# Optimization experiments

Hardware: AMD Instinct MI355X
Metric: run time of the kernel (lower is better)

The kernel has to match this reference:

```python
import jax, jax.numpy as jnp
import numpy as np

EMBED = 768
GH = 4        # heads per group
GD = 256      # group dim = GH * head_dim
NSTEPS = 3    # n_pde_steps
DT = 0.05
HJ_H = 0.05   # Heimburg-Jackson dispersion coefficient


def _sh(u, k):
    # shift field content along sequence axis (axis=1) by k with zero boundary
    if k == 0:
        return u
    z = jnp.zeros_like(u)
    if k > 0:
        return z.at[:, k:, :].set(u[:, :-k, :])
    return z.at[:, :k, :].set(u[:, -k:, :])


def _d1(u):
    return 0.5 * (_sh(u, -1) - _sh(u, 1))


def _d2(u):
    return _sh(u, -1) - 2.0 * u + _sh(u, 1)


def _d3(u):
    return 0.5 * (_sh(u, -2) - 2.0 * _sh(u, -1) + 2.0 * _sh(u, 1) - _sh(u, 2))


def _d4(u):
    return _sh(u, -2) - 4.0 * _sh(u, -1) + 6.0 * u - 4.0 * _sh(u, 1) + _sh(u, 2)


def _attn(x, qkv_w, qkv_b, ow, ob, nh):
    # standard causal multi-head attention on one head group
    B, T, D = x.shape
    hd = D // nh
    qkv = x @ qkv_w + qkv_b                      # (B,T,3D)
    q, k, v = jnp.split(qkv, 3, axis=-1)
    heads = lambda a: a.reshape(B, T, nh, hd).transpose(0, 2, 1, 3)
    q, k, v = heads(q), heads(k), heads(v)
    s = jnp.einsum('bhqd,bhkd->bhqk', q, k) * (1.0 / np.sqrt(hd))
    causal = jnp.tril(jnp.ones((T, T), dtype=bool))
    s = jnp.where(causal, s, jnp.asarray(-1e9, s.dtype))
    p = jax.nn.softmax(s, axis=-1)
    o = jnp.einsum('bhqk,bhkd->bhqd', p, v).transpose(0, 2, 1, 3).reshape(B, T, D)
    return o @ ow + ob


def _sine_gordon(u):
    # u_tt = u_xx - sin(u), semi-implicit Euler (leapfrog-like)
    w = jnp.zeros_like(u)
    for _ in range(NSTEPS):
        w = w + DT * (_d2(u) - jnp.sin(u))
        u = u + DT * w
    return u


def _kdv(u):
    # u_t = -6 u u_x - u_xxx, explicit Euler
    for _ in range(NSTEPS):
        u = u + DT * (-6.0 * u * _d1(u) - _d3(u))
    return u


def _hj(u):
    # Heimburg-Jackson: u_tt = d_xx((c0^2 + p u + q u^2) u) - h u_xxxx
    # with c0=1, p=-1, q=1
    w = jnp.zeros_like(u)
    for _ in range(NSTEPS):
        f = u - u * u + u * u * u
        w = w + DT * (_d2(f) - HJ_H * _d4(u))
        u = u + DT * w
    return u


def setup_inputs() -> dict:
    key = jax.random.key(0)
    ks = jax.random.split(key, 16)
    s = 0.02
    d, gd = EMBED, GD
    inp = {'x': jax.random.normal(ks[0], (4, 2048, d), dtype=jnp.float32)}
    inp['in_w'] = jax.random.normal(ks[1], (d, d), jnp.float32) * s
    inp['in_b'] = jnp.zeros((d,), jnp.float32)
    for i, n in enumerate(['sg', 'kdv', 'hj']):
        inp[n + '_qkv_w'] = jax.random.normal(ks[2 + 4 * i], (gd, 3 * gd), jnp.float32) * s
        inp[n + '_qkv_b'] = jnp.zeros((3 * gd,), jnp.float32)
        inp[n + '_out_w'] = jax.random.normal(ks[3 + 4 * i], (gd, gd), jnp.float32) * s
        inp[n + '_out_b'] = jnp.zeros((gd,), jnp.float32)
    inp['out_w'] = jax.random.normal(ks[14], (d, d), jnp.float32) * s
    inp['out_b'] = jnp.zeros((d,), jnp.float32)
    return inp


def reference(x, in_w, in_b,
              sg_qkv_w, sg_qkv_b, sg_out_w, sg_out_b,
              kdv_qkv_w, kdv_qkv_b, kdv_out_w, kdv_out_b,
              hj_qkv_w, hj_qkv_b, hj_out_w, hj_out_b,
              out_w, out_b):
    h = x @ in_w + in_b
    xg = jnp.split(h, [GD, 2 * GD], axis=-1)
    sg = _sine_gordon(_attn(xg[0], sg_qkv_w, sg_qkv_b, sg_out_w, sg_out_b, GH))
    kv = _kdv(_attn(xg[1], kdv_qkv_w, kdv_qkv_b, kdv_out_w, kdv_out_b, GH))
    hj = _hj(_attn(xg[2], hj_qkv_w, hj_qkv_b, hj_out_w, hj_out_b, GH))
    out = jnp.concatenate([sg, kv, hj], axis=-1)
    return out @ out_w + out_b
```

## Files before the change

kernel.cpp:

```cpp
#include <hip/hip_runtime.h>
#include <math.h>

#define B_   4
#define T_   2048
#define D_   768
#define M_   8192
#define GD_  256
#define NH_  4
#define HD_  64

typedef short  s16x8 __attribute__((ext_vector_type(8)));
typedef __bf16 bfx8  __attribute__((ext_vector_type(8)));
typedef float  fx4   __attribute__((ext_vector_type(4)));

#define LOG2E 1.44269504088896f
#define QSCALE (0.125f * LOG2E)

__device__ __forceinline__ short f2bf(float f) {
  union { float f; unsigned u; } v; v.f = f;
  unsigned r = v.u + 0x7fffu + ((v.u >> 16) & 1u);
  return (short)(r >> 16);
}

struct PW { const short* p0; const short* p1; const short* p2; };
struct PB { const float* p0; const float* p1; const float* p2; };
__device__ __forceinline__ const short* selw(const PW& s, int z) {
  return z == 0 ? s.p0 : (z == 1 ? s.p1 : s.p2);
}
__device__ __forceinline__ const float* selb(const PB& s, int z) {
  return z == 0 ? s.p0 : (z == 1 ? s.p1 : s.p2);
}

template<int AT, int OBF, int MODE>
__global__ __launch_bounds__(256) void gemm_mfma(
    const void* __restrict__ Avoid, long sA, int lda,
    PW Wp, PB Bp, int K,
    void* __restrict__ C, long sC, int ldc,
    void* __restrict__ xtra)
{
  __shared__ short As[128 * 72];
  __shared__ short Bs[64 * 72];

  const int z = blockIdx.z;
  const short* Ab16 = (const short*)Avoid + (long)z * sA;
  const float* Ab32 = (const float*)Avoid + (long)z * sA;
  const short* Wb = selw(Wp, z);
  const float* bb = selb(Bp, z);

  const int n0 = blockIdx.x * 64;
  const int m0 = blockIdx.y * 128;
  const int tid = threadIdx.x, lane = tid & 63, w = tid >> 6;
  const int wm = w >> 1, wn = w & 1;
  const int quad = lane >> 4, mr = lane & 15;

  const int r0 = tid >> 3;
  const int cs = (tid & 7) * 8;

  fx4 acc[4][2] = {};
  s16x8 ar[4], br[2];

  auto loadA = [&](int k0) {
#pragma unroll
    for (int gg = 0; gg < 4; ++gg) {
      if (AT) {
        const float* p = Ab32 + (long)(m0 + r0 + 32 * gg) * lda + k0 + cs;
        float4 f0 = *(const float4*)p;
        float4 f1 = *(const float4*)(p + 4);
        short o[8] = { f2bf(f0.x), f2bf(f0.y), f2bf(f0.z), f2bf(f0.w),
                       f2bf(f1.x), f2bf(f1.y), f2bf(f1.z), f2bf(f1.w) };
        ar[gg] = *(s16x8*)o;
      } else {
        ar[gg] = *(const s16x8*)(Ab16 + (long)(m0 + r0 + 32 * gg) * lda + k0 + cs);
      }
    }
  };
  auto loadB = [&](int k0) {
#pragma unroll
    for (int hh = 0; hh < 2; ++hh)
      br[hh] = *(const s16x8*)(Wb + (long)(n0 + r0 + 32 * hh) * K + k0 + cs);
  };

  loadA(0); loadB(0);

  for (int k0 = 0; k0 < K; k0 += 64) {
#pragma unroll
    for (int gg = 0; gg < 4; ++gg)
      *(s16x8*)&As[(r0 + 32 * gg) * 72 + cs] = ar[gg];
#pragma unroll
    for (int hh = 0; hh < 2; ++hh)
      *(s16x8*)&Bs[(r0 + 32 * hh) * 72 + cs] = br[hh];
    __syncthreads();

    if (k0 + 64 < K) { loadA(k0 + 64); loadB(k0 + 64); }

#pragma unroll
    for (int ks = 0; ks < 2; ++ks) {
      bfx8 af[4], bf[2];
#pragma unroll
      for (int i = 0; i < 4; ++i)
        af[i] = *(const bfx8*)&As[(wm * 64 + i * 16 + mr) * 72 + ks * 32 + quad * 8];
#pragma unroll
      for (int j = 0; j < 2; ++j)
        bf[j] = *(const bfx8*)&Bs[(wn * 32 + j * 16 + mr) * 72 + ks * 32 + quad * 8];
#pragma unroll
      for (int i = 0; i < 4; ++i)
#pragma unroll
        for (int j = 0; j < 2; ++j)
          acc[i][j] = __builtin_amdgcn_mfma_f32_16x16x32_bf16(af[i], bf[j], acc[i][j], 0, 0, 0);
    }
    __syncthreads();
  }

  float* Cf = (float*)C + (long)z * sC;
  short* Cs = (short*)C + (long)z * sC;
#pragma unroll
  for (int j = 0; j < 2; ++j) {
    const int col = n0 + wn * 32 + j * 16 + mr;
    const float bvx = bb[col];
#pragma unroll
    for (int i = 0; i < 4; ++i) {
      const int row0 = m0 + wm * 64 + i * 16 + quad * 4;
      if (MODE == 2) {
        const int rb = row0 >> 11, t0 = row0 & 2047;
        fx4 o;
#pragma unroll
        for (int r = 0; r < 4; ++r) o[r] = acc[i][j][r] + bvx;
        *(fx4*)((float*)xtra + (((long)z * B_ + rb) * GD_ + col) * T_ + t0) = o;
      } else if (MODE == 1 && col >= 512) {
        const int h = (col - 512) >> 6, hd = (col - 512) & 63;
        const int rb = row0 >> 11, t0 = row0 & 2047;
        short o4[4];
#pragma unroll
        for (int r = 0; r < 4; ++r) o4[r] = f2bf(acc[i][j][r] + bvx);
        *(short4*)((short*)xtra + ((((long)z * B_ + rb) * NH_ + h) * HD_ + hd) * T_ + t0) =
            *(short4*)o4;
      } else {
        const float sc = (MODE == 1 && col < 256) ? QSCALE : 1.0f;
#pragma unroll
        for (int r = 0; r < 4; ++r) {
          float v = (acc[i][j][r] + bvx) * sc;
          if (OBF) Cs[(long)(row0 + r) * ldc + col] = f2bf(v);
          else     Cf[(long)(row0 + r) * ldc + col] = v;
        }
      }
    }
  }
}

__global__ __launch_bounds__(256) void flash_attn_mfma(
    short* __restrict__ qkv, const short* __restrict__ vtb)
{
  __shared__ short Ks[64][72];
  __shared__ short Vs[80][72];
  __shared__ short Ps[128][72];

  const int bid = blockIdx.x;
  const int Q = 15 - (bid / 48);
  const int combo = bid % 48;
  const int g = combo % 3, bh = combo / 3;
  const int b = bh >> 2, h = bh & 3;

  short* base = qkv + ((size_t)g * M_ + (size_t)b * T_) * D_;
  short*       Qp = base + h * HD_;
  const short* Kp = base + GD_ + h * HD_;
  const short* Vtp = vtb + ((((size_t)g * B_ + b) * NH_ + h) * HD_) * T_;

  const int tid = threadIdx.x, lane = tid & 63, w = tid >> 6;
  const int quad = lane >> 4, mr = lane & 15;
  const int q0 = Q * 128, wr = w * 32;

  const int sra = tid >> 3, sc = (tid & 7) * 8;

  if (tid < 128) {
    const short ov = 0x3F80;
    s16x8 one = { ov, ov, ov, ov, ov, ov, ov, ov };
    *(s16x8*)&Vs[64 + (tid >> 3)][(tid & 7) * 8] = one;
  }

  bfx8 aq[2][2];
#pragma unroll
  for (int f = 0; f < 2; ++f)
#pragma unroll
    for (int ks = 0; ks < 2; ++ks)
      aq[f][ks] = *(const bfx8*)(Qp + (size_t)(q0 + wr + f * 16 + mr) * D_ +
                                 ks * 32 + quad * 8);

  s16x8 kreg0 = *(const s16x8*)(Kp + (size_t)sra * D_ + sc);
  s16x8 kreg1 = *(const s16x8*)(Kp + (size_t)(sra + 32) * D_ + sc);
  s16x8 vreg0 = *(const s16x8*)(Vtp + (size_t)sra * T_ + sc);
  s16x8 vreg1 = *(const s16x8*)(Vtp + (size_t)(sra + 32) * T_ + sc);

  fx4 Oa[2][5] = {};

  const int ktmax = 2 * Q + 1;
  for (int kt = 0; kt <= ktmax; ++kt) {
    *(s16x8*)&Ks[sra][sc]      = kreg0;
    *(s16x8*)&Ks[sra + 32][sc] = kreg1;
    *(s16x8*)&Vs[sra][sc]      = vreg0;
    *(s16x8*)&Vs[sra + 32][sc] = vreg1;
    __syncthreads();

    if (kt < ktmax) {
      const int kn = (kt + 1) * 64;
      kreg0 = *(const s16x8*)(Kp + (size_t)(kn + sra) * D_ + sc);
      kreg1 = *(const s16x8*)(Kp + (size_t)(kn + sra + 32) * D_ + sc);
      vreg0 = *(const s16x8*)(Vtp + (size_t)sra * T_ + kn + sc);
      vreg1 = *(const s16x8*)(Vtp + (size_t)(sra + 32) * T_ + kn + sc);
    }

    fx4 s[2][4] = {};
#pragma unroll
    for (int ks = 0; ks < 2; ++ks) {
      bfx8 bk[4];
#pragma unroll
      for (int j = 0; j < 4; ++j)
        bk[j] = *(const bfx8*)&Ks[j * 16 + mr][ks * 32 + quad * 8];
#pragma unroll
      for (int f = 0; f < 2; ++f)
#pragma unroll
        for (int j = 0; j < 4; ++j)
          s[f][j] = __builtin_amdgcn_mfma_f32_16x16x32_bf16(aq[f][ks], bk[j], s[f][j], 0, 0, 0);
    }

    if (kt >= 2 * Q) {
#pragma unroll
      for (int f = 0; f < 2; ++f)
#pragma unroll
        for (int j = 0; j < 4; ++j) {
          const int colg = kt * 64 + j * 16 + mr;
          const int rowg = q0 + wr + f * 16 + quad * 4;
#pragma unroll
          for (int r = 0; r < 4; ++r)
            if (colg > rowg + r) s[f][j][r] = -1e30f;
        }
    }

#pragma unroll
    for (int f = 0; f < 2; ++f)
#pragma unroll
      for (int j = 0; j < 4; ++j)
#pragma unroll
        for (int r = 0; r < 4; ++r)
          Ps[wr + f * 16 + quad * 4 + r][j * 16 + mr] = f2bf(exp2f(s[f][j][r]));

#pragma unroll
    for (int ks = 0; ks < 2; ++ks) {
      bfx8 ap[2];
#pragma unroll
      for (int f = 0; f < 2; ++f)
        ap[f] = *(const bfx8*)&Ps[wr + f * 16 + mr][ks * 32 + quad * 8];
#pragma unroll
      for (int j = 0; j < 5; ++j) {
        bfx8 bv = *(const bfx8*)&Vs[j * 16 + mr][ks * 32 + quad * 8];
#pragma unroll
        for (int f = 0; f < 2; ++f)
          Oa[f][j] = __builtin_amdgcn_mfma_f32_16x16x32_bf16(ap[f], bv, Oa[f][j], 0, 0, 0);
      }
    }
    __syncthreads();
  }

#pragma unroll
  for (int f = 0; f < 2; ++f)
#pragma unroll
    for (int r = 0; r < 4; ++r) {
      const float inv = 1.0f / Oa[f][4][r];
      const int row = q0 + wr + f * 16 + quad * 4 + r;
#pragma unroll
      for (int j = 0; j < 4; ++j)
        Qp[(size_t)row * D_ + j * 16 + mr] = f2bf(Oa[f][j][r] * inv);
    }
}

__device__ __forceinline__ float fhj(float x) { return x - x * x + x * x * x; }

__global__ __launch_bounds__(256) void pde_kernel(
    const float* __restrict__ ut, short* __restrict__ ub)
{
  __shared__ short ob[4][2056];

  const int cg = blockIdx.x, b = blockIdx.y, g = blockIdx.z;
  const int tid = threadIdx.x;
  const int c = tid >> 6, lane = tid & 63;
  const int t0 = lane * 32;
  const float dt = 0.05f;

  const float* src = ut + (((size_t)g * B_ + b) * GD_ + cg * 4 + c) * T_ + t0;

  float uc[36];
#pragma unroll
  for (int q = 0; q < 8; ++q)
    *(fx4*)&uc[2 + q * 4] = *(const fx4*)(src + q * 4);

  {
    float h0 = __shfl_up(uc[32], 1);
    float h1 = __shfl_up(uc[33], 1);
    float h2 = __shfl_down(uc[2], 1);
    float h3 = __shfl_down(uc[3], 1);
    uc[0]  = (lane == 0)  ? 0.f : h0;
    uc[1]  = (lane == 0)  ? 0.f : h1;
    uc[34] = (lane == 63) ? 0.f : h2;
    uc[35] = (lane == 63) ? 0.f : h3;
  }

  float wreg[32];
#pragma unroll
  for (int i = 0; i < 32; ++i) wreg[i] = 0.f;

  for (int step = 0; step < 3; ++step) {
    float nu[32];
#pragma unroll
    for (int tt = 0; tt < 32; ++tt) {
      float um2 = uc[tt], um1 = uc[tt + 1], u = uc[tt + 2];
      float up1 = uc[tt + 3], up2 = uc[tt + 4];
      if (g == 0) {
        float d2 = up1 - 2.f * u + um1;
        wreg[tt] += dt * (d2 - __sinf(u));
        nu[tt] = u + dt * wreg[tt];
      } else if (g == 1) {
        float d1 = 0.5f * (up1 - um1);
        float d3 = 0.5f * (up2 - 2.f * up1 + 2.f * um1 - um2);
        nu[tt] = u + dt * (-6.f * u * d1 - d3);
      } else {
        float d2f = fhj(up1) - 2.f * fhj(u) + fhj(um1);
        float d4  = up2 - 4.f * up1 + 6.f * u - 4.f * um1 + um2;
        wreg[tt] += dt * (d2f - 0.05f * d4);
        nu[tt] = u + dt * wreg[tt];
      }
    }
    float h0 = __shfl_up(nu[30], 1);
    float h1 = __shfl_up(nu[31], 1);
    float h2 = __shfl_down(nu[0], 1);
    float h3 = __shfl_down(nu[1], 1);
    uc[0]  = (lane == 0)  ? 0.f : h0;
    uc[1]  = (lane == 0)  ? 0.f : h1;
    uc[34] = (lane == 63) ? 0.f : h2;
    uc[35] = (lane == 63) ? 0.f : h3;
#pragma unroll
    for (int i = 0; i < 32; ++i) uc[2 + i] = nu[i];
  }

  short o16[32];
#pragma unroll
  for (int i = 0; i < 32; ++i) o16[i] = f2bf(uc[2 + i]);
#pragma unroll
  for (int q = 0; q < 4; ++q)
    *(s16x8*)&ob[c][t0 + q * 8] = *(s16x8*)&o16[q * 8];
  __syncthreads();

  short* dst = ub + (size_t)b * T_ * D_ + g * GD_ + cg * 4;
#pragma unroll
  for (int q = 0; q < 8; ++q) {
    int t = tid + q * 256;
    short o4[4];
#pragma unroll
    for (int cc = 0; cc < 4; ++cc) o4[cc] = ob[cc][t];
    *(short4*)(dst + (size_t)t * D_) = *(short4*)o4;
  }
}

struct PrepArgs {
  const float* w[8]; short* wt[8];
  int K[8], N[8];
  int tend[8];
};

__global__ __launch_bounds__(256) void prep_kernel(PrepArgs pa)
{
  const int bid = blockIdx.x, tid = threadIdx.x;
  __shared__ float Ws[32][33];
  int ti = 0;
#pragma unroll
  for (int i = 0; i < 8; ++i) if (bid >= pa.tend[i]) ti = i + 1;
  const int tloc = bid - (ti ? pa.tend[ti - 1] : 0);
  const int K = pa.K[ti], N = pa.N[ti];
  const int ntx = N >> 5;
  const int k0 = (tloc / ntx) * 32, n0 = (tloc % ntx) * 32;
  const float* W = pa.w[ti];
  short* WT = pa.wt[ti];
  const int tx = tid & 31, ty = tid >> 5;

#pragma unroll
  for (int i = 0; i < 4; ++i)
    Ws[ty + 8 * i][tx] = W[(long)(k0 + ty + 8 * i) * N + n0 + tx];
  __syncthreads();
#pragma unroll
  for (int i = 0; i < 4; ++i) {
    int r = ty + 8 * i;
    WT[(long)(n0 + r) * K + k0 + tx] = f2bf(Ws[tx][r]);
  }
}

extern "C" void kernel_launch(void* const* d_in, const int* in_sizes, int n_in,
                              void* d_out, int out_size, void* d_ws, size_t ws_size,
                              hipStream_t stream)
{
  (void)in_sizes; (void)n_in; (void)out_size; (void)ws_size;

  const float* x         = (const float*)d_in[0];
  const float* in_w      = (const float*)d_in[1];
  const float* in_b      = (const float*)d_in[2];
  const float* sg_qkv_w  = (const float*)d_in[3];
  const float* sg_qkv_b  = (const float*)d_in[4];
  const float* sg_out_w  = (const float*)d_in[5];
  const float* sg_out_b  = (const float*)d_in[6];
  const float* kdv_qkv_w = (const float*)d_in[7];
  const float* kdv_qkv_b = (const float*)d_in[8];
  const float* kdv_out_w = (const float*)d_in[9];
  const float* kdv_out_b = (const float*)d_in[10];
  const float* hj_qkv_w  = (const float*)d_in[11];
  const float* hj_qkv_b  = (const float*)d_in[12];
  const float* hj_out_w  = (const float*)d_in[13];
  const float* hj_out_b  = (const float*)d_in[14];
  const float* out_w     = (const float*)d_in[15];
  const float* out_b     = (const float*)d_in[16];
  float* out = (float*)d_out;

  const size_t MD = (size_t)M_ * D_;
  short* base = (short*)d_ws;
  short* hb   = base + MD;
  float* uf   = (float*)d_ws;
  short* qkvb = base + 2 * MD;
  short* ub16 = qkvb + 3 * MD;
  short* wts  = ub16 + MD;
  short* in_wT  = wts;
  short* qkvT0  = in_wT + 589824;
  short* qkvT1  = qkvT0 + 196608;
  short* qkvT2  = qkvT1 + 196608;
  short* outT0  = qkvT2 + 196608;
  short* outT1  = outT0 + 65536;
  short* outT2  = outT1 + 65536;
  short* out_wT = outT2 + 65536;
  short* vtb    = out_wT + 589824;

  dim3 blk(256);

  PrepArgs pa;
  const float* wsrc[8] = { in_w, sg_qkv_w, kdv_qkv_w, hj_qkv_w,
                           sg_out_w, kdv_out_w, hj_out_w, out_w };
  short* wdst[8] = { in_wT, qkvT0, qkvT1, qkvT2, outT0, outT1, outT2, out_wT };
  int Ksz[8] = { 768, 256, 256, 256, 256, 256, 256, 768 };
  int Nsz[8] = { 768, 768, 768, 768, 256, 256, 256, 768 };
  int cum = 0;
  for (int i = 0; i < 8; ++i) {
    pa.w[i] = wsrc[i]; pa.wt[i] = wdst[i]; pa.K[i] = Ksz[i]; pa.N[i] = Nsz[i];
    cum += (Ksz[i] >> 5) * (Nsz[i] >> 5);
    pa.tend[i] = cum;
  }
  prep_kernel<<<dim3((unsigned)cum), blk, 0, stream>>>(pa);

  gemm_mfma<1, 1, 0><<<dim3(12, 64, 1), blk, 0, stream>>>(
      x, 0, D_, PW{in_wT, in_wT, in_wT}, PB{in_b, in_b, in_b}, D_,
      hb, 0, D_, nullptr);

  gemm_mfma<0, 1, 1><<<dim3(12, 64, 3), blk, 0, stream>>>(
      hb, 256, D_,
      PW{qkvT0, qkvT1, qkvT2}, PB{sg_qkv_b, kdv_qkv_b, hj_qkv_b}, GD_,
      qkvb, (long)MD, D_, vtb);

  flash_attn_mfma<<<dim3(768), blk, 0, stream>>>(qkvb, vtb);

  gemm_mfma<0, 0, 2><<<dim3(4, 64, 3), blk, 0, stream>>>(
      qkvb, (long)MD, D_,
      PW{outT0, outT1, outT2}, PB{sg_out_b, kdv_out_b, hj_out_b}, GD_,
      uf, 0, 0, uf);

  pde_kernel<<<dim3(64, 4, 3), blk, 0, stream>>>(uf, ub16);

  gemm_mfma<0, 0, 0><<<dim3(12, 64, 1), blk, 0, stream>>>(
      ub16, 0, D_, PW{out_wT, out_wT, out_wT}, PB{out_b, out_b, out_b}, D_,
      out, 0, D_, nullptr);
}
```

Before: 313.3 us.

## Transpose QK^T MFMA, pack bf16 P stores with XOR swizzle, skip masked tiles per wave

Computes S^T by swapping the MFMA operands, so each lane holds four consecutive key positions for one query row. This lets the exp'd probabilities be packed with v_cvt_pk_bf16_f32 and written to the P tile as 8-byte stores into an XOR-swizzled LDS layout, replacing scattered 2-byte stores with software rounding. Each wave also skips the whole QK/PV compute for key tiles lying entirely above its own 32 query rows. The cost is added swizzle address arithmetic and inline asm that depends on the target ISA.

```diff
diff --git a/kernel.cpp b/kernel.cpp
--- a/kernel.cpp
+++ b/kernel.cpp
@@ -20,6 +20,12 @@
   union { float f; unsigned u; } v; v.f = f;
   unsigned r = v.u + 0x7fffu + ((v.u >> 16) & 1u);
   return (short)(r >> 16);
+}
+
+__device__ __forceinline__ unsigned cvt_pk_bf16(float lo, float hi) {
+  unsigned r;
+  asm("v_cvt_pk_bf16_f32 %0, %1, %2" : "=v"(r) : "v"(lo), "v"(hi));
+  return r;
 }
 
 struct PW { const short* p0; const short* p1; const short* p2; };
@@ -168,6 +174,7 @@
   const int tid = threadIdx.x, lane = tid & 63, w = tid >> 6;
   const int quad = lane >> 4, mr = lane & 15;
   const int q0 = Q * 128, wr = w * 32;
+  const int qhi = q0 + wr + 31;
 
   const int sra = tid >> 3, sc = (tid & 7) * 8;
 
@@ -191,6 +198,9 @@
   s16x8 vreg1 = *(const s16x8*)(Vtp + (size_t)(sra + 32) * T_ + sc);
 
   fx4 Oa[2][5] = {};
+
+  char* PsB = (char*)&Ps[0][0];
+  const int xorb = (mr & 7) << 4;
 
   const int ktmax = 2 * Q + 1;
   for (int kt = 0; kt <= ktmax; ++kt) {
@@ -208,53 +218,68 @@
       vreg1 = *(const s16x8*)(Vtp + (size_t)(sra + 32) * T_ + kn + sc);
     }
 
-    fx4 s[2][4] = {};
-#pragma unroll
-    for (int ks = 0; ks < 2; ++ks) {
-      bfx8 bk[4];
-#pragma unroll
-      for (int j = 0; j < 4; ++j)
-        bk[j] = *(const bfx8*)&Ks[j * 16 + mr][ks * 32 + quad * 8];
-#pragma unroll
-      for (int f = 0; f < 2; ++f)
-#pragma unroll
-        for (int j = 0; j < 4; ++j)
-          s[f][j] = __builtin_amdgcn_mfma_f32_16x16x32_bf16(aq[f][ks], bk[j], s[f][j], 0, 0, 0);
-    }
-
-    if (kt >= 2 * Q) {
-#pragma unroll
-      for (int f = 0; f < 2; ++f)
-#pragma unroll
-        for (int j = 0; j < 4; ++j) {
-          const int colg = kt * 64 + j * 16 + mr;
-          const int rowg = q0 + wr + f * 16 + quad * 4;
-#pragma unroll
-          for (int r = 0; r < 4; ++r)
-            if (colg > rowg + r) s[f][j][r] = -1e30f;
+    if (kt * 64 <= qhi) {
+      fx4 st[4][2] = {};
+#pragma unroll
+      for (int ks = 0; ks < 2; ++ks) {
+        bfx8 bk[4];
+#pragma unroll
+        for (int jj = 0; jj < 4; ++jj)
+          bk[jj] = *(const bfx8*)&Ks[jj * 16 + mr][ks * 32 + quad * 8];
+#pragma unroll
+        for (int jj = 0; jj < 4; ++jj)
+#pragma unroll
+          for (int f = 0; f < 2; ++f)
+            st[jj][f] = __builtin_amdgcn_mfma_f32_16x16x32_bf16(bk[jj], aq[f][ks], st[jj][f], 0, 0, 0);
+      }
+
+      if (kt >= 2 * Q) {
+#pragma unroll
+        for (int jj = 0; jj < 4; ++jj)
+#pragma unroll
+          for (int f = 0; f < 2; ++f) {
+            const int qg = q0 + wr + f * 16 + mr;
+            const int kvg0 = kt * 64 + jj * 16 + quad * 4;
+#pragma unroll
+            for (int r = 0; r < 4; ++r)
+              if (kvg0 + r > qg) st[jj][f][r] = -1e30f;
+          }
+      }
+
+#pragma unroll
+      for (int f = 0; f < 2; ++f) {
+        const long rowb = (long)(wr + f * 16 + mr) * 144;
+#pragma unroll
+        for (int jj = 0; jj < 4; ++jj) {
+          float e0 = exp2f(st[jj][f][0]);
+          float e1 = exp2f(st[jj][f][1]);
+          float e2 = exp2f(st[jj][f][2]);
+          float e3 = exp2f(st[jj][f][3]);
+          unsigned pk0 = cvt_pk_bf16(e0, e1);
+          unsigned pk1 = cvt_pk_bf16(e2, e3);
+          unsigned long long pv = (unsigned long long)pk0 |
+                                  ((unsigned long long)pk1 << 32);
+          const int kb = (jj * 32 + quad * 8) ^ xorb;
+          *(unsigned long long*)(PsB + rowb + kb) = pv;
         }
-    }
-
-#pragma unroll
-    for (int f = 0; f < 2; ++f)
-#pragma unroll
-      for (int j = 0; j < 4; ++j)
-#pragma unroll
-        for (int r = 0; r < 4; ++r)
-          Ps[wr + f * 16 + quad * 4 + r][j * 16 + mr] = f2bf(exp2f(s[f][j][r]));
-
-#pragma unroll
-    for (int ks = 0; ks < 2; ++ks) {
-      bfx8 ap[2];
-#pragma unroll
-      for (int f = 0; f < 2; ++f)
-        ap[f] = *(const bfx8*)&Ps[wr + f * 16 + mr][ks * 32 + quad * 8];
-#pragma unroll
-      for (int j = 0; j < 5; ++j) {
-        bfx8 bv = *(const bfx8*)&Vs[j * 16 + mr][ks * 32 + quad * 8];
-#pragma unroll
-        for (int f = 0; f < 2; ++f)
-          Oa[f][j] = __builtin_amdgcn_mfma_f32_16x16x32_bf16(ap[f], bv, Oa[f][j], 0, 0, 0);
+      }
+
+#pragma unroll
+      for (int ks = 0; ks < 2; ++ks) {
+        bfx8 ap[2];
+#pragma unroll
+        for (int f = 0; f < 2; ++f) {
+          const long rowb = (long)(wr + f * 16 + mr) * 144;
+          const int kb = (ks * 64 + quad * 16) ^ xorb;
+          ap[f] = *(const bfx8*)(PsB + rowb + kb);
+        }
+#pragma unroll
+        for (int j = 0; j < 5; ++j) {
+          bfx8 bv = *(const bfx8*)&Vs[j * 16 + mr][ks * 32 + quad * 8];
+#pragma unroll
+          for (int f = 0; f < 2; ++f)
+            Oa[f][j] = __builtin_amdgcn_mfma_f32_16x16x32_bf16(ap[f], bv, Oa[f][j], 0, 0, 0);
+        }
       }
     }
     __syncthreads();
```

Result: no change. 314.1 us (+0.2%).
